# Kernel tuning notes

Hardware: AMD Instinct MI355X
Metric: run time of the kernel (lower is better)

## Reference

```python
import jax, jax.numpy as jnp
import numpy as np

EPS = 1e-12  # matches torch F.normalize default eps

def setup_inputs() -> dict:
    key = jax.random.key(0)
    k1, k2 = jax.random.split(key)
    n, d = 8192, 1024
    x = jax.random.normal(k1, (n, d), dtype=jnp.float32)
    weight = jax.random.normal(k2, (d, d), dtype=jnp.float32) * (2.0 / d) ** 0.5
    return {"x": x, "weight": weight}

def reference(x, weight):
    # L2-normalize rows (torch F.normalize, dim=1): x / max(||x||_2, eps)
    nrm = jnp.sqrt(jnp.sum(x * x, axis=1, keepdims=True))
    norm = x / jnp.maximum(nrm, EPS)
    # adjacency: cosine-similarity Gram matrix [n, n] (materialized as in source)
    adj = norm @ norm.T
    ax = adj @ x          # [n, d]
    axw = ax @ weight     # [n, d]
    return axw
```

## Files before the change

kernel.cpp:

```cpp
#include <hip/hip_runtime.h>
#include <stdint.h>

typedef unsigned short u16;
typedef unsigned int u32;
typedef __attribute__((ext_vector_type(8))) short short8;
typedef __attribute__((ext_vector_type(4))) float floatx4;

__device__ __forceinline__ u16 f2b(float f) {
    u32 u = __builtin_bit_cast(u32, f);
    return (u16)((u + 0x7fffu + ((u >> 16) & 1u)) >> 16);
}

__device__ __forceinline__ void gld16(const void* g, void* l) {
    __builtin_amdgcn_global_load_lds(
        (const __attribute__((address_space(1))) u32*)g,
        (__attribute__((address_space(3))) u32*)l, 16, 0, 0);
}

__global__ __launch_bounds__(256) void prep_all(
    const float* __restrict__ x, const float* __restrict__ wgt,
    u16* __restrict__ YT, u16* __restrict__ Yn, u16* __restrict__ Wt) {
    __shared__ __align__(16) float sh[64 * 66];
    int b = blockIdx.x;
    int t = threadIdx.x;
    if (b < 256) {
        float (*tile)[129] = (float(*)[129])sh;
        int r0 = b * 32;
        int tg = t >> 5, tl = t & 31;
        float ss[4] = {0.f, 0.f, 0.f, 0.f};
        for (int c = 0; c < 8; c++) {
            #pragma unroll
            for (int i = 0; i < 4; i++) {
                int rr = i * 8 + tg;
                float4 v = *(const float4*)(x + (long)(r0 + rr) * 1024 + c * 128 + tl * 4);
                ss[i] += v.x * v.x + v.y * v.y + v.z * v.z + v.w * v.w;
            }
        }
        float rs_[4], sr_[4];
        #pragma unroll
        for (int i = 0; i < 4; i++) {
            #pragma unroll
            for (int m = 16; m > 0; m >>= 1) ss[i] += __shfl_xor(ss[i], m);
            float rcp = 1.0f / fmaxf(sqrtf(ss[i]), 1e-12f);
            rs_[i] = rcp;
            sr_[i] = sqrtf(rcp);
        }
        for (int c = 0; c < 8; c++) {
            __syncthreads();
            #pragma unroll
            for (int i = 0; i < 4; i++) {
                int rr = i * 8 + tg;
                float4 v = *(const float4*)(x + (long)(r0 + rr) * 1024 + c * 128 + tl * 4);
                ushort4 o;
                o.x = f2b(v.x * rs_[i]); o.y = f2b(v.y * rs_[i]);
                o.z = f2b(v.z * rs_[i]); o.w = f2b(v.w * rs_[i]);
                *(ushort4*)(Yn + (long)(r0 + rr) * 1024 + c * 128 + tl * 4) = o;
                tile[rr][tl * 4 + 0] = v.x * sr_[i];
                tile[rr][tl * 4 + 1] = v.y * sr_[i];
                tile[rr][tl * 4 + 2] = v.z * sr_[i];
                tile[rr][tl * 4 + 3] = v.w * sr_[i];
            }
            __syncthreads();
            #pragma unroll
            for (int i = 0; i < 4; i++) {
                int lin = i * 256 + t;
                int cc = lin >> 3, r4 = (lin & 7) << 2;
                ushort4 o;
                o.x = f2b(tile[r4 + 0][cc]); o.y = f2b(tile[r4 + 1][cc]);
                o.z = f2b(tile[r4 + 2][cc]); o.w = f2b(tile[r4 + 3][cc]);
                *(ushort4*)(YT + (long)(c * 128 + cc) * 8192 + r0 + r4) = o;
            }
        }
    } else {
        float (*tile)[65] = (float(*)[65])sh;
        int bb = b - 256;
        int r0 = (bb >> 4) * 64, c0 = (bb & 15) * 64;
        #pragma unroll
        for (int i = 0; i < 4; i++) {
            int lin = i * 256 + t;
            int rr = lin >> 4, c4 = (lin & 15) << 2;
            float4 v = *(const float4*)(wgt + (long)(r0 + rr) * 1024 + c0 + c4);
            tile[rr][c4] = v.x; tile[rr][c4 + 1] = v.y;
            tile[rr][c4 + 2] = v.z; tile[rr][c4 + 3] = v.w;
        }
        __syncthreads();
        #pragma unroll
        for (int i = 0; i < 4; i++) {
            int lin = i * 256 + t;
            int cc = lin >> 4, r4 = (lin & 15) << 2;
            ushort4 o;
            o.x = f2b(tile[r4][cc]);
            o.y = f2b(tile[r4 + 1][cc]);
            o.z = f2b(tile[r4 + 2][cc]);
            o.w = f2b(tile[r4 + 3][cc]);
            *(ushort4*)(Wt + (long)(c0 + cc) * 1024 + r0 + r4) = o;
        }
    }
}

__global__ __launch_bounds__(256) void reduce_symC(
    const float* __restrict__ P, u16* __restrict__ D, int S, long E) {
    __shared__ float lt[64][65];
    int ti = blockIdx.x >> 4, tj = blockIdx.x & 15;
    if (ti > 2 * (tj >> 1) + 1) return;
    int mir = (tj > 2 * (ti >> 1) + 1);
    int t = threadIdx.x;
    int r = t >> 4, c4 = (t & 15) << 2;
    #pragma unroll
    for (int it = 0; it < 4; it++) {
        int row = it * 16 + r;
        long idx = (long)(64 * ti + row) * 1024 + 64 * tj + c4;
        float4 s = *(const float4*)(P + idx);
        for (int z = 1; z < S; z++) {
            float4 v = *(const float4*)(P + (long)z * E + idx);
            s.x += v.x; s.y += v.y; s.z += v.z; s.w += v.w;
        }
        ushort4 o; o.x = f2b(s.x); o.y = f2b(s.y); o.z = f2b(s.z); o.w = f2b(s.w);
        *(ushort4*)(D + idx) = o;
        if (mir) {
            lt[row][c4] = s.x; lt[row][c4 + 1] = s.y;
            lt[row][c4 + 2] = s.z; lt[row][c4 + 3] = s.w;
        }
    }
    if (mir) {
        __syncthreads();
        #pragma unroll
        for (int it = 0; it < 4; it++) {
            int dr = it * 16 + r;
            ushort4 o;
            o.x = f2b(lt[c4 + 0][dr]); o.y = f2b(lt[c4 + 1][dr]);
            o.z = f2b(lt[c4 + 2][dr]); o.w = f2b(lt[c4 + 3][dr]);
            *(ushort4*)(D + (long)(64 * tj + dr) * 1024 + 64 * ti + c4) = o;
        }
    }
}

__global__ __launch_bounds__(256, 3) void gemm64x128(
    const u16* __restrict__ A, const u16* __restrict__ B,
    float* __restrict__ C, const float* __restrict__ rowscale,
    int lda, int ldb, int ldc, int tilesN, int kIters, long coffz, int sym, int obf16) {
    __shared__ __align__(16) u16 As[64 * 128];
    __shared__ __align__(16) u16 Bs[128 * 128];
    int bid = blockIdx.x;
    int nx = gridDim.x;
    if ((nx & 7) == 0) { int cpx = nx >> 3; bid = (bid & 7) * cpx + (bid >> 3); }
    int tm, tn;
    if (sym) {
        int id = bid, j = 0;
        while (true) {
            int c = (2 * j + 2 < 16) ? (2 * j + 2) : 16;
            if (id < c) break;
            id -= c; j++;
        }
        tn = j; tm = id;
    } else {
        tm = bid / tilesN; tn = bid % tilesN;
    }
    long kOff = (long)blockIdx.y * kIters * 128;
    const u16* Ap = A + (long)tm * 64 * lda + kOff;
    const u16* Bp = B + (long)tn * 128 * ldb + kOff;
    long coff = (long)blockIdx.y * coffz;

    int t = threadIdx.x;
    int lane = t & 63, w = t >> 6;
    int wm = (w & 1) * 32, wn = (w >> 1) * 64;
    int r16 = lane & 15, q = lane >> 4;

    floatx4 acc[2][4];
    #pragma unroll
    for (int i = 0; i < 2; i++)
        #pragma unroll
        for (int j = 0; j < 4; j++) acc[i][j] = (floatx4){0.f, 0.f, 0.f, 0.f};

    for (int kt = 0; kt < kIters; kt++) {
        long kk = (long)kt * 128;
        #pragma unroll
        for (int j = 0; j < 4; j++) {
            int cl = j * 256 + t, row = cl >> 4, cg = (cl & 15) ^ (row & 15);
            gld16(Ap + (long)row * lda + kk + cg * 8, (void*)&As[cl * 8]);
        }
        #pragma unroll
        for (int j = 0; j < 8; j++) {
            int cl = j * 256 + t, row = cl >> 4, cg = (cl & 15) ^ (row & 15);
            gld16(Bp + (long)row * ldb + kk + cg * 8, (void*)&Bs[cl * 8]);
        }
        __syncthreads();
        #pragma unroll
        for (int ks = 0; ks < 4; ks++) {
            short8 a[2], b[4];
            #pragma unroll
            for (int i = 0; i < 2; i++) {
                int rr = wm + i * 16 + r16;
                int cc = (ks * 4 + q) ^ (rr & 15);
                a[i] = *(const short8*)&As[rr * 128 + cc * 8];
            }
            #pragma unroll
            for (int j = 0; j < 4; j++) {
                int rr = wn + j * 16 + r16;
                int cc = (ks * 4 + q) ^ (rr & 15);
                b[j] = *(const short8*)&Bs[rr * 128 + cc * 8];
            }
            #pragma unroll
            for (int i = 0; i < 2; i++)
                #pragma unroll
                for (int j = 0; j < 4; j++)
                    acc[i][j] = __builtin_amdgcn_mfma_f32_16x16x32_bf16(a[i], b[j], acc[i][j], 0, 0, 0);
        }
        __syncthreads();
    }

    int m0 = tm * 64 + wm, n0 = tn * 128 + wn;
    #pragma unroll
    for (int i = 0; i < 2; i++) {
        int mm = m0 + i * 16 + q * 4;
        float rs[4];
        #pragma unroll
        for (int r = 0; r < 4; r++) rs[r] = (rowscale != nullptr) ? rowscale[mm + r] : 1.0f;
        #pragma unroll
        for (int j = 0; j < 4; j++) {
            int nn = n0 + j * 16 + r16;
            #pragma unroll
            for (int r = 0; r < 4; r++) {
                float v = acc[i][j][r] * rs[r];
                if (obf16) ((u16*)C)[coff + (long)(mm + r) * ldc + nn] = f2b(v);
                else       C[coff + (long)(mm + r) * ldc + nn] = v;
            }
        }
    }
}

__global__ __launch_bounds__(256, 2) void gemm128(
    const u16* __restrict__ A, const u16* __restrict__ B,
    float* __restrict__ C, const float* __restrict__ rowscale,
    int lda, int ldb, int ldc, int tilesN, int kIters) {
    __shared__ __align__(16) u16 As[128 * 128];
    __shared__ __align__(16) u16 Bs[128 * 128];
    int bid = blockIdx.x;
    int nx = gridDim.x;
    if ((nx & 7) == 0) { int cpx = nx >> 3; bid = (bid & 7) * cpx + (bid >> 3); }
    int tm = bid / tilesN, tn = bid % tilesN;
    const u16* Ap = A + (long)tm * 128 * lda;
    const u16* Bp = B + (long)tn * 128 * ldb;

    int t = threadIdx.x;
    int lane = t & 63, w = t >> 6;
    int wm = (w & 1) * 64, wn = (w >> 1) * 64;
    int r16 = lane & 15, q = lane >> 4;

    floatx4 acc[4][4];
    #pragma unroll
    for (int i = 0; i < 4; i++)
        #pragma unroll
        for (int j = 0; j < 4; j++) acc[i][j] = (floatx4){0.f, 0.f, 0.f, 0.f};

    for (int kt = 0; kt < kIters; kt++) {
        long kk = (long)kt * 128;
        #pragma unroll
        for (int j = 0; j < 8; j++) {
            int cl = j * 256 + t, row = cl >> 4, cg = (cl & 15) ^ (row & 15);
            gld16(Ap + (long)row * lda + kk + cg * 8, (void*)&As[cl * 8]);
        }
        #pragma unroll
        for (int j = 0; j < 8; j++) {
            int cl = j * 256 + t, row = cl >> 4, cg = (cl & 15) ^ (row & 15);
            gld16(Bp + (long)row * ldb + kk + cg * 8, (void*)&Bs[cl * 8]);
        }
        __syncthreads();
        #pragma unroll
        for (int ks = 0; ks < 4; ks++) {
            short8 a[4], b[4];
            #pragma unroll
            for (int i = 0; i < 4; i++) {
                int rr = wm + i * 16 + r16;
                int cc = (ks * 4 + q) ^ (rr & 15);
                a[i] = *(const short8*)&As[rr * 128 + cc * 8];
            }
            #pragma unroll
            for (int j = 0; j < 4; j++) {
                int rr = wn + j * 16 + r16;
                int cc = (ks * 4 + q) ^ (rr & 15);
                b[j] = *(const short8*)&Bs[rr * 128 + cc * 8];
            }
            #pragma unroll
            for (int i = 0; i < 4; i++)
                #pragma unroll
                for (int j = 0; j < 4; j++)
                    acc[i][j] = __builtin_amdgcn_mfma_f32_16x16x32_bf16(a[i], b[j], acc[i][j], 0, 0, 0);
        }
        __syncthreads();
    }

    int m0 = tm * 128 + wm, n0 = tn * 128 + wn;
    #pragma unroll
    for (int i = 0; i < 4; i++) {
        int mm = m0 + i * 16 + q * 4;
        float rs[4];
        #pragma unroll
        for (int r = 0; r < 4; r++) rs[r] = (rowscale != nullptr) ? rowscale[mm + r] : 1.0f;
        #pragma unroll
        for (int j = 0; j < 4; j++) {
            int nn = n0 + j * 16 + r16;
            #pragma unroll
            for (int r = 0; r < 4; r++)
                C[(long)(mm + r) * ldc + nn] = acc[i][j][r] * rs[r];
        }
    }
}

extern "C" void kernel_launch(void* const* d_in, const int* in_sizes, int n_in,
                              void* d_out, int out_size, void* d_ws, size_t ws_size,
                              hipStream_t stream) {
    const float* x = (const float*)d_in[0];
    const float* wgt = (const float*)d_in[1];
    float* out = (float*)d_out;
    char* ws = (char*)d_ws;

    const size_t MB = 1048576;
    u16*   YT = (u16*)ws;
    u16*   Yn = (u16*)(ws + 16 * MB);
    u16*   Wt = (u16*)(ws + 32 * MB);
    u16*   Gb = (u16*)(ws + 34 * MB);
    u16*   Mt = (u16*)(ws + 36 * MB);
    float* Gp = (float*)(ws + 38 * MB);

    prep_all<<<512, 256, 0, stream>>>(x, wgt, YT, Yn, Wt);
    gemm64x128<<<dim3(72, 8), 256, 0, stream>>>(YT, YT, Gp, nullptr,
                                                8192, 8192, 1024, 8, 8, 1048576, 1, 0);
    reduce_symC<<<256, 256, 0, stream>>>(Gp, Gb, 8, 1048576);
    gemm64x128<<<dim3(128, 1), 256, 0, stream>>>(Wt, Gb, (float*)Mt, nullptr,
                                                 1024, 1024, 1024, 8, 8, 0, 0, 1);
    gemm128<<<dim3(512, 1), 256, 0, stream>>>(Yn, Mt, out, nullptr,
                                              1024, 1024, 1024, 8, 8);
}
```

Baseline: 162.3 us.

## Double-buffer LDS tiles with K=64 stages in both GEMM kernels

```diff
diff --git a/kernel.cpp b/kernel.cpp
--- a/kernel.cpp
+++ b/kernel.cpp
@@ -139,8 +139,8 @@
     const u16* __restrict__ A, const u16* __restrict__ B,
     float* __restrict__ C, const float* __restrict__ rowscale,
     int lda, int ldb, int ldc, int tilesN, int kIters, long coffz, int sym, int obf16) {
-    __shared__ __align__(16) u16 As[64 * 128];
-    __shared__ __align__(16) u16 Bs[128 * 128];
+    __shared__ __align__(16) u16 As[2][64 * 64];
+    __shared__ __align__(16) u16 Bs[2][128 * 64];
     int bid = blockIdx.x;
     int nx = gridDim.x;
     if ((nx & 7) == 0) { int cpx = nx >> 3; bid = (bid & 7) * cpx + (bid >> 3); }
@@ -156,7 +156,7 @@
     } else {
         tm = bid / tilesN; tn = bid % tilesN;
     }
-    long kOff = (long)blockIdx.y * kIters * 128;
+    long kOff = (long)blockIdx.y * kIters * 64;
     const u16* Ap = A + (long)tm * 64 * lda + kOff;
     const u16* Bp = B + (long)tn * 128 * ldb + kOff;
     long coff = (long)blockIdx.y * coffz;
@@ -166,48 +166,69 @@
     int wm = (w & 1) * 32, wn = (w >> 1) * 64;
     int r16 = lane & 15, q = lane >> 4;
 
+    int acl[2], bcl[4];
+    #pragma unroll
+    for (int j = 0; j < 2; j++) acl[j] = (w * 2 + j) * 64 + lane;
+    #pragma unroll
+    for (int j = 0; j < 4; j++) bcl[j] = (w * 4 + j) * 64 + lane;
+
     floatx4 acc[2][4];
     #pragma unroll
     for (int i = 0; i < 2; i++)
         #pragma unroll
         for (int j = 0; j < 4; j++) acc[i][j] = (floatx4){0.f, 0.f, 0.f, 0.f};
 
-    for (int kt = 0; kt < kIters; kt++) {
-        long kk = (long)kt * 128;
-        #pragma unroll
-        for (int j = 0; j < 4; j++) {
-            int cl = j * 256 + t, row = cl >> 4, cg = (cl & 15) ^ (row & 15);
-            gld16(Ap + (long)row * lda + kk + cg * 8, (void*)&As[cl * 8]);
-        }
-        #pragma unroll
-        for (int j = 0; j < 8; j++) {
-            int cl = j * 256 + t, row = cl >> 4, cg = (cl & 15) ^ (row & 15);
-            gld16(Bp + (long)row * ldb + kk + cg * 8, (void*)&Bs[cl * 8]);
-        }
+    #define STAGE64(buf, kt)                                                    \
+        {                                                                       \
+            long kk = (long)(kt) * 64;                                          \
+            _Pragma("unroll")                                                   \
+            for (int j = 0; j < 2; j++) {                                       \
+                int cl = acl[j], row = cl >> 3, cg = (cl & 7) ^ (row & 7);      \
+                gld16(Ap + (long)row * lda + kk + cg * 8, (void*)&As[buf][cl * 8]); \
+            }                                                                   \
+            _Pragma("unroll")                                                   \
+            for (int j = 0; j < 4; j++) {                                       \
+                int cl = bcl[j], row = cl >> 3, cg = (cl & 7) ^ (row & 7);      \
+                gld16(Bp + (long)row * ldb + kk + cg * 8, (void*)&Bs[buf][cl * 8]); \
+            }                                                                   \
+        }
+
+    #define COMPUTE64(buf)                                                      \
+        {                                                                       \
+            _Pragma("unroll")                                                   \
+            for (int ks = 0; ks < 2; ks++) {                                    \
+                short8 a[2], b[4];                                              \
+                _Pragma("unroll")                                               \
+                for (int i = 0; i < 2; i++) {                                   \
+                    int rr = wm + i * 16 + r16;                                 \
+                    int cc = (ks * 4 + q) ^ (rr & 7);                           \
+                    a[i] = *(const short8*)&As[buf][rr * 64 + cc * 8];          \
+                }                                                               \
+                _Pragma("unroll")                                               \
+                for (int j = 0; j < 4; j++) {                                   \
+                    int rr = wn + j * 16 + r16;                                 \
+                    int cc = (ks * 4 + q) ^ (rr & 7);                           \
+                    b[j] = *(const short8*)&Bs[buf][rr * 64 + cc * 8];          \
+                }                                                               \
+                _Pragma("unroll")                                               \
+                for (int i = 0; i < 2; i++)                                     \
+                    _Pragma("unroll")                                           \
+                    for (int j = 0; j < 4; j++)                                 \
+                        acc[i][j] = __builtin_amdgcn_mfma_f32_16x16x32_bf16(    \
+                            a[i], b[j], acc[i][j], 0, 0, 0);                    \
+            }                                                                   \
+        }
+
+    STAGE64(0, 0);
+    __syncthreads();
+    int cur = 0;
+    for (int kt = 0; kt < kIters - 1; kt++) {
+        STAGE64(cur ^ 1, kt + 1);
+        COMPUTE64(cur);
         __syncthreads();
-        #pragma unroll
-        for (int ks = 0; ks < 4; ks++) {
-            short8 a[2], b[4];
-            #pragma unroll
-            for (int i = 0; i < 2; i++) {
-                int rr = wm + i * 16 + r16;
-                int cc = (ks * 4 + q) ^ (rr & 15);
-                a[i] = *(const short8*)&As[rr * 128 + cc * 8];
-            }
-            #pragma unroll
-            for (int j = 0; j < 4; j++) {
-                int rr = wn + j * 16 + r16;
-                int cc = (ks * 4 + q) ^ (rr & 15);
-                b[j] = *(const short8*)&Bs[rr * 128 + cc * 8];
-            }
-            #pragma unroll
-            for (int i = 0; i < 2; i++)
-                #pragma unroll
-                for (int j = 0; j < 4; j++)
-                    acc[i][j] = __builtin_amdgcn_mfma_f32_16x16x32_bf16(a[i], b[j], acc[i][j], 0, 0, 0);
-        }
-        __syncthreads();
-    }
+        cur ^= 1;
+    }
+    COMPUTE64(cur);
 
     int m0 = tm * 64 + wm, n0 = tn * 128 + wn;
     #pragma unroll
@@ -227,14 +248,16 @@
             }
         }
     }
+    #undef STAGE64
+    #undef COMPUTE64
 }
 
 __global__ __launch_bounds__(256, 2) void gemm128(
     const u16* __restrict__ A, const u16* __restrict__ B,
     float* __restrict__ C, const float* __restrict__ rowscale,
     int lda, int ldb, int ldc, int tilesN, int kIters) {
-    __shared__ __align__(16) u16 As[128 * 128];
-    __shared__ __align__(16) u16 Bs[128 * 128];
+    __shared__ __align__(16) u16 As[2][128 * 64];
+    __shared__ __align__(16) u16 Bs[2][128 * 64];
     int bid = blockIdx.x;
     int nx = gridDim.x;
     if ((nx & 7) == 0) { int cpx = nx >> 3; bid = (bid & 7) * cpx + (bid >> 3); }
@@ -253,42 +276,57 @@
         #pragma unroll
         for (int j = 0; j < 4; j++) acc[i][j] = (floatx4){0.f, 0.f, 0.f, 0.f};
 
-    for (int kt = 0; kt < kIters; kt++) {
-        long kk = (long)kt * 128;
-        #pragma unroll
-        for (int j = 0; j < 8; j++) {
-            int cl = j * 256 + t, row = cl >> 4, cg = (cl & 15) ^ (row & 15);
-            gld16(Ap + (long)row * lda + kk + cg * 8, (void*)&As[cl * 8]);
-        }
-        #pragma unroll
-        for (int j = 0; j < 8; j++) {
-            int cl = j * 256 + t, row = cl >> 4, cg = (cl & 15) ^ (row & 15);
-            gld16(Bp + (long)row * ldb + kk + cg * 8, (void*)&Bs[cl * 8]);
-        }
+    #define STAGE128(buf, kt)                                                   \
+        {                                                                       \
+            long kk = (long)(kt) * 64;                                          \
+            _Pragma("unroll")                                                   \
+            for (int j = 0; j < 4; j++) {                                       \
+                int cl = j * 256 + t, row = cl >> 3, cg = (cl & 7) ^ (row & 7); \
+                gld16(Ap + (long)row * lda + kk + cg * 8, (void*)&As[buf][cl * 8]); \
+            }                                                                   \
+            _Pragma("unroll")                                                   \
+            for (int j = 0; j < 4; j++) {                                       \
+                int cl = j * 256 + t, row = cl >> 3, cg = (cl & 7) ^ (row & 7); \
+                gld16(Bp + (long)row * ldb + kk + cg * 8, (void*)&Bs[buf][cl * 8]); \
+            }                                                                   \
+        }
+
+    #define COMPUTE128(buf)                                                     \
+        {                                                                       \
+            _Pragma("unroll")                                                   \
+            for (int ks = 0; ks < 2; ks++) {                                    \
+                short8 a[4], b[4];                                              \
+                _Pragma("unroll")                                               \
+                for (int i = 0; i < 4; i++) {                                   \
+                    int rr = wm + i * 16 + r16;                                 \
+                    int cc = (ks * 4 + q) ^ (rr & 7);                           \
+                    a[i] = *(const short8*)&As[buf][rr * 64 + cc * 8];          \
+                }                                                               \
+                _Pragma("unroll")                                               \
+                for (int j = 0; j < 4; j++) {                                   \
+                    int rr = wn + j * 16 + r16;                                 \
+                    int cc = (ks * 4 + q) ^ (rr & 7);                           \
+                    b[j] = *(const short8*)&Bs[buf][rr * 64 + cc * 8];          \
+                }                                                               \
+                _Pragma("unroll")                                               \
+                for (int i = 0; i < 4; i++)                                     \
+                    _Pragma("unroll")                                           \
+                    for (int j = 0; j < 4; j++)                                 \
+                        acc[i][j] = __builtin_amdgcn_mfma_f32_16x16x32_bf16(    \
+                            a[i], b[j], acc[i][j], 0, 0, 0);                    \
+            }                                                                   \
+        }
+
+    STAGE128(0, 0);
+    __syncthreads();
+    int cur = 0;
+    for (int kt = 0; kt < kIters - 1; kt++) {
+        STAGE128(cur ^ 1, kt + 1);
+        COMPUTE128(cur);
         __syncthreads();
-        #pragma unroll
-        for (int ks = 0; ks < 4; ks++) {
-            short8 a[4], b[4];
-            #pragma unroll
-            for (int i = 0; i < 4; i++) {
-                int rr = wm + i * 16 + r16;
-                int cc = (ks * 4 + q) ^ (rr & 15);
-                a[i] = *(const short8*)&As[rr * 128 + cc * 8];
-            }
-            #pragma unroll
-            for (int j = 0; j < 4; j++) {
-                int rr = wn + j * 16 + r16;
-                int cc = (ks * 4 + q) ^ (rr & 15);
-                b[j] = *(const short8*)&Bs[rr * 128 + cc * 8];
-            }
-            #pragma unroll
-            for (int i = 0; i < 4; i++)
-                #pragma unroll
-                for (int j = 0; j < 4; j++)
-                    acc[i][j] = __builtin_amdgcn_mfma_f32_16x16x32_bf16(a[i], b[j], acc[i][j], 0, 0, 0);
-        }
-        __syncthreads();
-    }
+        cur ^= 1;
+    }
+    COMPUTE128(cur);
 
     int m0 = tm * 128 + wm, n0 = tn * 128 + wn;
     #pragma unroll
@@ -305,6 +343,8 @@
                 C[(long)(mm + r) * ldc + nn] = acc[i][j][r] * rs[r];
         }
     }
+    #undef STAGE128
+    #undef COMPUTE128
 }
 
 extern "C" void kernel_launch(void* const* d_in, const int* in_sizes, int n_in,
@@ -325,10 +365,10 @@
 
     prep_all<<<512, 256, 0, stream>>>(x, wgt, YT, Yn, Wt);
     gemm64x128<<<dim3(72, 8), 256, 0, stream>>>(YT, YT, Gp, nullptr,
-                                                8192, 8192, 1024, 8, 8, 1048576, 1, 0);
+                                                8192, 8192, 1024, 8, 16, 1048576, 1, 0);
     reduce_symC<<<256, 256, 0, stream>>>(Gp, Gb, 8, 1048576);
     gemm64x128<<<dim3(128, 1), 256, 0, stream>>>(Wt, Gb, (float*)Mt, nullptr,
-                                                 1024, 1024, 1024, 8, 8, 0, 0, 1);
+                                                 1024, 1024, 1024, 8, 16, 0, 0, 1);
     gemm128<<<dim3(512, 1), 256, 0, stream>>>(Yn, Mt, out, nullptr,
-                                              1024, 1024, 1024, 8, 8);
-}
+                                              1024, 1024, 1024, 8, 16);
+}
```

Result: slower. 169.7 us (+4.6%).
